# Kernel tuning notes

Hardware: AMD Instinct MI355X
Metric: run time of the kernel (lower is better)

## Reference

```python
import jax, jax.numpy as jnp
import numpy as np

B, T = 2, 2048
D_MODEL = 1024
N_LAYERS = 2
VOCAB = 256
BLOCK = 2048
LOCAL = 128
STRIDE = 256
NHEAD = D_MODEL // 64  # 16
HEAD_DIM = D_MODEL // NHEAD  # 64
LN_EPS = 1e-5


def setup_inputs() -> dict:
    key = jax.random.key(0)
    ks = jax.random.split(key, 16)
    L, d = N_LAYERS, D_MODEL

    def g(k, shape, scale=0.02):
        return (jax.random.normal(k, shape, dtype=jnp.float32) * scale)

    return {
        "x": jax.random.randint(ks[0], (B, T), 0, VOCAB),
        "embed": g(ks[1], (VOCAB, d)),
        "pos_embed": g(ks[2], (BLOCK, d)),
        # per-layer weights stacked on leading L axis; Linear as y = x @ W + b
        "Wq": g(ks[3], (L, d, d)), "bq": jnp.zeros((L, d), jnp.float32),
        "Wk": g(ks[4], (L, d, d)), "bk": jnp.zeros((L, d), jnp.float32),
        "Wv": g(ks[5], (L, d, d)), "bv": jnp.zeros((L, d), jnp.float32),
        "Wo": g(ks[6], (L, d, d)), "bo": jnp.zeros((L, d), jnp.float32),
        "g1": jnp.ones((L, d), jnp.float32), "be1": jnp.zeros((L, d), jnp.float32),
        "W1": g(ks[7], (L, d, 4 * d)), "bf1": jnp.zeros((L, 4 * d), jnp.float32),
        "W2": g(ks[8], (L, 4 * d, d)), "bf2": jnp.zeros((L, d), jnp.float32),
        "g2": jnp.ones((L, d), jnp.float32), "be2": jnp.zeros((L, d), jnp.float32),
        "gf": jnp.ones((d,), jnp.float32), "bef": jnp.zeros((d,), jnp.float32),
        "Whead": g(ks[9], (d, VOCAB)),
    }


def _ln(x, gamma, beta):
    mu = jnp.mean(x, axis=-1, keepdims=True)
    var = jnp.mean(jnp.square(x - mu), axis=-1, keepdims=True)
    return (x - mu) * jax.lax.rsqrt(var + LN_EPS) * gamma + beta


def _sparse_mask(t):
    # allowed[i, j] = True if token i may attend to token j
    i = jnp.arange(t)[:, None]
    j = jnp.arange(t)[None, :]
    causal = j <= i
    local = (i - j) <= LOCAL
    glob = (j % STRIDE) == 0
    return causal & (local | glob)


def _sparse_attn(q, k, v, allowed):
    # q, k, v: [B, T, D] -> [B, H, T, hd]
    b, t, d = q.shape
    def split(x):
        return x.reshape(b, t, NHEAD, HEAD_DIM).transpose(0, 2, 1, 3)
    q, k, v = split(q), split(k), split(v)
    scale = HEAD_DIM ** -0.5
    scores = jnp.einsum("bhqd,bhkd->bhqk", q, k) * scale
    scores = jnp.where(allowed[None, None], scores, -jnp.inf)
    attn = jax.nn.softmax(scores, axis=-1)  # every row has j=i allowed -> no NaN
    out = jnp.einsum("bhqk,bhkd->bhqd", attn, v)
    return out.transpose(0, 2, 1, 3).reshape(b, t, d)


def reference(x, embed, pos_embed, Wq, bq, Wk, bk, Wv, bv, Wo, bo,
              g1, be1, W1, bf1, W2, bf2, g2, be2, gf, bef, Whead):
    b, t = x.shape
    h = embed[x] + pos_embed[jnp.arange(t)][None]
    allowed = _sparse_mask(t)
    for l in range(N_LAYERS):
        h_n = _ln(h, g1[l], be1[l])
        q = h_n @ Wq[l] + bq[l]
        k = h_n @ Wk[l] + bk[l]
        v = h_n @ Wv[l] + bv[l]
        attn_out = _sparse_attn(q, k, v, allowed)
        h = h + (attn_out @ Wo[l] + bo[l])
        h2 = _ln(h, g2[l], be2[l])
        ffn = jax.nn.gelu(h2 @ W1[l] + bf1[l], approximate=False) @ W2[l] + bf2[l]
        h = h + ffn
    h = _ln(h, gf, bef)
    return h @ Whead
```

## Files before the change

### kernel.cpp

```cpp
#include <hip/hip_runtime.h>
#include <hip/hip_bf16.h>

#define BB 2
#define TT 2048
#define DD 1024
#define FF 4096
#define VV 256
#define HH 16
#define HD 64
#define MM (BB * TT)
#define LOCAL_W 128
#define STRIDE_G 256
#define QS 3072

typedef short s16x8 __attribute__((ext_vector_type(8)));
typedef __bf16 bf16x8 __attribute__((ext_vector_type(8)));
typedef float f32x4 __attribute__((ext_vector_type(4)));

#define WAITVM(N) asm volatile("s_waitcnt vmcnt(" #N ")" ::: "memory")
#define LGKM0 do { asm volatile("s_waitcnt lgkmcnt(0)" ::: "memory"); \
                   __builtin_amdgcn_sched_barrier(0); } while (0)

__device__ __forceinline__ float b2f(unsigned short u) {
  return __builtin_bit_cast(float, (unsigned int)u << 16);
}
__device__ __forceinline__ unsigned short f2b(float f) {
  __hip_bfloat16 h = __float2bfloat16(f);
  return __builtin_bit_cast(unsigned short, h);
}
__device__ __forceinline__ void gl_lds16(const unsigned short* g, unsigned short* l) {
  __builtin_amdgcn_global_load_lds(
      (const __attribute__((address_space(1))) void*)g,
      (__attribute__((address_space(3))) void*)l, 16, 0, 0);
}
__device__ __forceinline__ bf16x8 ldsr(const unsigned short* p) {
  return __builtin_bit_cast(bf16x8, *(const s16x8*)p);
}

__global__ __launch_bounds__(256) void transpose_k(const float* __restrict__ W,
                                                   unsigned short* __restrict__ WT,
                                                   int K, int N) {
  __shared__ float t[32][33];
  const int n0 = blockIdx.x * 32, k0 = blockIdx.y * 32;
  const int tx = threadIdx.x, ty = threadIdx.y;
  for (int r = ty; r < 32; r += 8) t[r][tx] = W[(size_t)(k0 + r) * N + n0 + tx];
  __syncthreads();
  for (int r = ty; r < 32; r += 8)
    WT[(size_t)(n0 + r) * K + k0 + tx] = f2b(t[tx][r]);
}

__global__ __launch_bounds__(256) void concat_bias(const float* __restrict__ bq,
                                                   const float* __restrict__ bk,
                                                   const float* __restrict__ bv,
                                                   float* __restrict__ bcat) {
  const int i = blockIdx.x * 256 + threadIdx.x;
  const int l = i / QS, j = i - l * QS;
  float v;
  if (j < DD) v = bq[l * DD + j];
  else if (j < 2 * DD) v = bk[l * DD + j - DD];
  else v = bv[l * DD + j - 2 * DD];
  bcat[i] = v;
}

__global__ __launch_bounds__(256) void embed_kernel(const int* __restrict__ x,
                                                    const float* __restrict__ emb,
                                                    const float* __restrict__ pos,
                                                    float* __restrict__ h) {
  const int row = blockIdx.x;
  const int c = threadIdx.x * 4;
  const int tok = x[row];
  const int t = row & (TT - 1);
  float4 e = *(const float4*)&emb[(size_t)tok * DD + c];
  float4 p = *(const float4*)&pos[(size_t)t * DD + c];
  e.x += p.x; e.y += p.y; e.z += p.z; e.w += p.w;
  *(float4*)&h[(size_t)row * DD + c] = e;
}

__global__ __launch_bounds__(256) void ln_kernel(const float* __restrict__ x,
                                                 const float* __restrict__ g,
                                                 const float* __restrict__ be,
                                                 unsigned short* __restrict__ out) {
  const int row = blockIdx.x;
  const int tid = threadIdx.x;
  const float4 v = *(const float4*)&x[(size_t)row * DD + tid * 4];
  float s = v.x + v.y + v.z + v.w;
  float sq = v.x * v.x + v.y * v.y + v.z * v.z + v.w * v.w;
#pragma unroll
  for (int off = 32; off; off >>= 1) {
    s += __shfl_xor(s, off);
    sq += __shfl_xor(sq, off);
  }
  __shared__ float ss[4], ssq[4];
  const int w = tid >> 6, lane = tid & 63;
  if (lane == 0) { ss[w] = s; ssq[w] = sq; }
  __syncthreads();
  s = ss[0] + ss[1] + ss[2] + ss[3];
  sq = ssq[0] + ssq[1] + ssq[2] + ssq[3];
  const float mean = s * (1.0f / DD);
  const float var = sq * (1.0f / DD) - mean * mean;
  const float rstd = rsqrtf(var + 1e-5f);
  const float4 gv = *(const float4*)&g[tid * 4];
  const float4 bv = *(const float4*)&be[tid * 4];
  ushort4 o;
  o.x = f2b((v.x - mean) * rstd * gv.x + bv.x);
  o.y = f2b((v.y - mean) * rstd * gv.y + bv.y);
  o.z = f2b((v.z - mean) * rstd * gv.z + bv.z);
  o.w = f2b((v.w - mean) * rstd * gv.w + bv.w);
  *(ushort4*)&out[(size_t)row * DD + tid * 4] = o;
}

__global__ __launch_bounds__(256) void ln_red(float* __restrict__ hio,
                                              const float* __restrict__ parts,
                                              const float* __restrict__ bias,
                                              const float* __restrict__ g,
                                              const float* __restrict__ be,
                                              unsigned short* __restrict__ out) {
  const int row = blockIdx.x;
  const int tid = threadIdx.x;
  const size_t base = (size_t)row * DD + tid * 4;
  f32x4 v = *(const f32x4*)&hio[base];
  v += *(const f32x4*)&bias[tid * 4];
  v += *(const f32x4*)&parts[base];
  v += *(const f32x4*)&parts[(size_t)MM * DD + base];
  *(f32x4*)&hio[base] = v;
  float s = v[0] + v[1] + v[2] + v[3];
  float sq = v[0] * v[0] + v[1] * v[1] + v[2] * v[2] + v[3] * v[3];
#pragma unroll
  for (int off = 32; off; off >>= 1) {
    s += __shfl_xor(s, off);
    sq += __shfl_xor(sq, off);
  }
  __shared__ float ss[4], ssq[4];
  const int w = tid >> 6, lane = tid & 63;
  if (lane == 0) { ss[w] = s; ssq[w] = sq; }
  __syncthreads();
  s = ss[0] + ss[1] + ss[2] + ss[3];
  sq = ssq[0] + ssq[1] + ssq[2] + ssq[3];
  const float mean = s * (1.0f / DD);
  const float var = sq * (1.0f / DD) - mean * mean;
  const float rstd = rsqrtf(var + 1e-5f);
  const float4 gv = *(const float4*)&g[tid * 4];
  const float4 bv = *(const float4*)&be[tid * 4];
  ushort4 o;
  o.x = f2b((v[0] - mean) * rstd * gv.x + bv.x);
  o.y = f2b((v[1] - mean) * rstd * gv.y + bv.y);
  o.z = f2b((v[2] - mean) * rstd * gv.z + bv.z);
  o.w = f2b((v[3] - mean) * rstd * gv.w + bv.w);
  *(ushort4*)&out[(size_t)row * DD + tid * 4] = o;
}

template <int EPI>
__global__ __launch_bounds__(512, 2) void gemm8p(const unsigned short* __restrict__ A,
                                                 const unsigned short* __restrict__ BT,
                                                 const float* __restrict__ bias,
                                                 unsigned short* __restrict__ outp,
                                                 int M, int N, int K, int nbx) {
  __shared__ __align__(16) unsigned short lds[65536];
  const int tid = threadIdx.x;
  const int lane = tid & 63;
  const int w = tid >> 6;
  const int nwg = gridDim.x;
  const int orig = blockIdx.x;
  const int wg = (orig & 7) * (nwg >> 3) + (orig >> 3);
  const int n0 = (wg % nbx) * 256, m0 = (wg / nbx) * 256;
  const int wm = w >> 2, wn = w & 3;
  f32x4 acc[8][4] = {};

  const unsigned short* aSrc[2];
  const unsigned short* bSrc[2];
  int dstO[2];
#pragma unroll
  for (int i = 0; i < 2; i++) {
    const int s = tid + (i << 9);
    const int row = s >> 2, sc = s & 3;
    const int l = sc ^ ((row >> 1) & 3);
    aSrc[i] = &A[(size_t)(m0 + row) * K + l * 8];
    bSrc[i] = &BT[(size_t)(n0 + row) * K + l * 8];
    dstO[i] = s * 8;
  }
  auto STAGE = [&](int tb, int ks, int obase) {
    const int kt = (tb << 6) + (ks << 5);
    const int so = obase + ks * 16384;
#pragma unroll
    for (int i = 0; i < 2; i++) {
      gl_lds16(aSrc[i] + kt, &lds[so + dstO[i]]);
      gl_lds16(bSrc[i] + kt, &lds[so + 8192 + dstO[i]]);
    }
  };

  const int rA = lane & 15, cr = lane >> 4;
  const int rowA0 = wm * 128 + rA;
  const int rowB0 = wn * 64 + rA;
  const int aAddr0 = rowA0 * 32 + ((cr ^ ((rowA0 >> 1) & 3)) << 3);
  const int bAddr0 = 8192 + rowB0 * 32 + ((cr ^ ((rowB0 >> 1) & 3)) << 3);

  const int NT = K >> 6;
  STAGE(0, 0, 0);
  STAGE(0, 1, 0);

  auto TILE = [&](int bufc, int tb, bool notlast) {
    const int bb = bufc << 15;
    const int ob = (bufc ^ 1) << 15;
    bf16x8 bfr[4], af[4];
    WAITVM(4);
    __builtin_amdgcn_s_barrier();
#pragma unroll
    for (int n = 0; n < 4; n++) bfr[n] = ldsr(&lds[bb + bAddr0 + n * 512]);
#pragma unroll
    for (int i = 0; i < 4; i++) af[i] = ldsr(&lds[bb + aAddr0 + i * 512]);
    if (notlast) STAGE(tb + 1, 0, ob);
    LGKM0;
    __builtin_amdgcn_s_setprio(1);
#pragma unroll
    for (int i = 0; i < 4; i++)
#pragma unroll
      for (int n = 0; n < 4; n++)
        acc[i][n] = __builtin_amdgcn_mfma_f32_16x16x32_bf16(af[i], bfr[n], acc[i][n], 0, 0, 0);
    __builtin_amdgcn_s_setprio(0);
#pragma unroll
    for (int i = 0; i < 4; i++) af[i] = ldsr(&lds[bb + aAddr0 + (4 + i) * 512]);
    LGKM0;
    __builtin_amdgcn_s_setprio(1);
#pragma unroll
    for (int i = 0; i < 4; i++)
#pragma unroll
      for (int n = 0; n < 4; n++)
        acc[4 + i][n] = __builtin_amdgcn_mfma_f32_16x16x32_bf16(af[i], bfr[n], acc[4 + i][n], 0, 0, 0);
    __builtin_amdgcn_s_setprio(0);
    if (notlast) { WAITVM(4); } else { WAITVM(0); }
    __builtin_amdgcn_s_barrier();
#pragma unroll
    for (int n = 0; n < 4; n++) bfr[n] = ldsr(&lds[bb + 16384 + bAddr0 + n * 512]);
#pragma unroll
    for (int i = 0; i < 4; i++) af[i] = ldsr(&lds[bb + 16384 + aAddr0 + i * 512]);
    if (notlast) STAGE(tb + 1, 1, ob);
    LGKM0;
    __builtin_amdgcn_s_setprio(1);
#pragma unroll
    for (int i = 0; i < 4; i++)
#pragma unroll
      for (int n = 0; n < 4; n++)
        acc[i][n] = __builtin_amdgcn_mfma_f32_16x16x32_bf16(af[i], bfr[n], acc[i][n], 0, 0, 0);
    __builtin_amdgcn_s_setprio(0);
#pragma unroll
    for (int i = 0; i < 4; i++) af[i] = ldsr(&lds[bb + 16384 + aAddr0 + (4 + i) * 512]);
    LGKM0;
    __builtin_amdgcn_s_setprio(1);
#pragma unroll
    for (int i = 0; i < 4; i++)
#pragma unroll
      for (int n = 0; n < 4; n++)
        acc[4 + i][n] = __builtin_amdgcn_mfma_f32_16x16x32_bf16(af[i], bfr[n], acc[4 + i][n], 0, 0, 0);
    __builtin_amdgcn_s_setprio(0);
  };

  for (int it = 0; it < NT; it += 2) {
    TILE(0, it, true);
    TILE(1, it + 1, it + 2 < NT);
  }

  const int r0 = (lane >> 4) * 4;
  const int cc = lane & 15;
#pragma unroll
  for (int m = 0; m < 8; m++) {
#pragma unroll
    for (int n = 0; n < 4; n++) {
#pragma unroll
      for (int r = 0; r < 4; r++) {
        const int row = m0 + wm * 128 + m * 16 + r0 + r;
        const int col = n0 + wn * 64 + n * 16 + cc;
        float val = acc[m][n][r] + bias[col];
        if (EPI == 3) {
          float u = val * (0.7978845608f + 0.0356774081f * val * val);
          u = fminf(u, 10.0f);
          const float e = __expf(2.0f * u);
          val = val * e / (e + 1.0f);
        }
        outp[(size_t)row * N + col] = f2b(val);
      }
    }
  }
}

__global__ __launch_bounds__(512, 2) void gemm_dw(const unsigned short* __restrict__ A,
                                                  const unsigned short* __restrict__ BT,
                                                  float* __restrict__ partial,
                                                  int M, int N, int K, int nbx, int nwg2,
                                                  int ksub) {
  __shared__ __align__(16) unsigned short lds[49152];
  const int tid = threadIdx.x;
  const int lane = tid & 63;
  const int w = tid >> 6;
  const int nwg = gridDim.x;
  const int orig = blockIdx.x;
  const int wg = (orig & 7) * (nwg >> 3) + (orig >> 3);
  const int ks = wg / nwg2;
  const int rem = wg - ks * nwg2;
  const int n0 = (rem % nbx) * 128;
  const int m0 = (rem / nbx) * 256;
  const int kb = ks * ksub;
  const int wm = w >> 2, wn = w & 3;
  f32x4 acc[8][2] = {};

  const unsigned short* aSrc[2];
  const unsigned short* bSrc;
  int dstA[2], dstB;
#pragma unroll
  for (int i = 0; i < 2; i++) {
    const int s = tid + (i << 9);
    const int row = s >> 2, sc = s & 3;
    const int l = sc ^ ((row >> 1) & 3);
    aSrc[i] = &A[(size_t)(m0 + row) * K + kb + l * 8];
    dstA[i] = s * 8;
  }
  {
    const int row = tid >> 2, sc = tid & 3;
    const int l = sc ^ ((row >> 1) & 3);
    bSrc = &BT[(size_t)(n0 + row) * K + kb + l * 8];
    dstB = 8192 + tid * 8;
  }
  auto STAGE = [&](int tb, int kss, int obase) {
    const int kt = (tb << 6) + (kss << 5);
    const int so = obase + kss * 12288;
    gl_lds16(aSrc[0] + kt, &lds[so + dstA[0]]);
    gl_lds16(aSrc[1] + kt, &lds[so + dstA[1]]);
    gl_lds16(bSrc + kt, &lds[so + dstB]);
  };

  const int rA = lane & 15, cr = lane >> 4;
  const int rowA0 = wm * 128 + rA;
  const int rowB0 = wn * 32 + rA;
  const int aAddr0 = rowA0 * 32 + ((cr ^ ((rowA0 >> 1) & 3)) << 3);
  const int bAddr0 = 8192 + rowB0 * 32 + ((cr ^ ((rowB0 >> 1) & 3)) << 3);

  const int NT = ksub >> 6;
  STAGE(0, 0, 0);
  STAGE(0, 1, 0);

  auto TILE = [&](int bufc, int tb, bool notlast) {
    const int bb = bufc * 24576;
    const int ob = (bufc ^ 1) * 24576;
    bf16x8 bfr[2], af[4];
    WAITVM(3);
    __builtin_amdgcn_s_barrier();
#pragma unroll
    for (int n = 0; n < 2; n++) bfr[n] = ldsr(&lds[bb + bAddr0 + n * 512]);
#pragma unroll
    for (int i = 0; i < 4; i++) af[i] = ldsr(&lds[bb + aAddr0 + i * 512]);
    if (notlast) STAGE(tb + 1, 0, ob);
    LGKM0;
    __builtin_amdgcn_s_setprio(1);
#pragma unroll
    for (int i = 0; i < 4; i++)
#pragma unroll
      for (int n = 0; n < 2; n++)
        acc[i][n] = __builtin_amdgcn_mfma_f32_16x16x32_bf16(af[i], bfr[n], acc[i][n], 0, 0, 0);
    __builtin_amdgcn_s_setprio(0);
#pragma unroll
    for (int i = 0; i < 4; i++) af[i] = ldsr(&lds[bb + aAddr0 + (4 + i) * 512]);
    LGKM0;
    __builtin_amdgcn_s_setprio(1);
#pragma unroll
    for (int i = 0; i < 4; i++)
#pragma unroll
      for (int n = 0; n < 2; n++)
        acc[4 + i][n] = __builtin_amdgcn_mfma_f32_16x16x32_bf16(af[i], bfr[n], acc[4 + i][n], 0, 0, 0);
    __builtin_amdgcn_s_setprio(0);
    if (notlast) { WAITVM(3); } else { WAITVM(0); }
    __builtin_amdgcn_s_barrier();
#pragma unroll
    for (int n = 0; n < 2; n++) bfr[n] = ldsr(&lds[bb + 12288 + bAddr0 + n * 512]);
#pragma unroll
    for (int i = 0; i < 4; i++) af[i] = ldsr(&lds[bb + 12288 + aAddr0 + i * 512]);
    if (notlast) STAGE(tb + 1, 1, ob);
    LGKM0;
    __builtin_amdgcn_s_setprio(1);
#pragma unroll
    for (int i = 0; i < 4; i++)
#pragma unroll
      for (int n = 0; n < 2; n++)
        acc[i][n] = __builtin_amdgcn_mfma_f32_16x16x32_bf16(af[i], bfr[n], acc[i][n], 0, 0, 0);
    __builtin_amdgcn_s_setprio(0);
#pragma unroll
    for (int i = 0; i < 4; i++) af[i] = ldsr(&lds[bb + 12288 + aAddr0 + (4 + i) * 512]);
    LGKM0;
    __builtin_amdgcn_s_setprio(1);
#pragma unroll
    for (int i = 0; i < 4; i++)
#pragma unroll
      for (int n = 0; n < 2; n++)
        acc[4 + i][n] = __builtin_amdgcn_mfma_f32_16x16x32_bf16(af[i], bfr[n], acc[4 + i][n], 0, 0, 0);
    __builtin_amdgcn_s_setprio(0);
  };

  for (int it = 0; it < NT; it += 2) {
    TILE(0, it, true);
    TILE(1, it + 1, it + 2 < NT);
  }

  float* pout = partial + (size_t)ks * M * N;
  const int r0 = (lane >> 4) * 4;
  const int cc = lane & 15;
#pragma unroll
  for (int m = 0; m < 8; m++)
#pragma unroll
    for (int n = 0; n < 2; n++)
#pragma unroll
      for (int r = 0; r < 4; r++) {
        const int row = m0 + wm * 128 + m * 16 + r0 + r;
        const int col = n0 + wn * 32 + n * 16 + cc;
        pout[(size_t)row * N + col] = acc[m][n][r];
      }
}

template <int EPI>
__global__ __launch_bounds__(512, 2) void gemm_p(const unsigned short* __restrict__ A,
                                                 const unsigned short* __restrict__ BT,
                                                 const float* __restrict__ bias,
                                                 const float* __restrict__ res,
                                                 void* __restrict__ outp,
                                                 int M, int N, int K, int nbx, int nwg2,
                                                 int ksub) {
  constexpr int BM = 128;
  __shared__ __align__(16) unsigned short lds[4][BM * 64];
  const int tid = threadIdx.x;
  const int lane = tid & 63;
  const int w = tid >> 6;
  const int nwg = gridDim.x;
  const int orig = blockIdx.x;
  const int wg = (orig & 7) * (nwg >> 3) + (orig >> 3);
  const int ks = wg / nwg2;
  const int rem = wg - ks * nwg2;
  const int n0 = (rem % nbx) * BM;
  const int m0 = (rem / nbx) * BM;
  const int kb = ks * ksub;
  const int wm = w >> 2, wn = w & 3;
  f32x4 acc[4][2] = {};

  auto STAGE = [&](int t) {
    const int b = t & 3;
    const int kt = kb + (t << 5);
    const int s = tid;
    const int row = s >> 2, sc = s & 3;
    const int c = sc ^ ((row >> 1) & 3);
    gl_lds16(&A[(size_t)(m0 + row) * K + kt + c * 8], &lds[b][s * 8]);
    gl_lds16(&BT[(size_t)(n0 + row) * K + kt + c * 8], &lds[b][BM * 32 + s * 8]);
  };

  const int NT = ksub >> 5;
  STAGE(0); STAGE(1); STAGE(2);

  for (int t = 0; t < NT; ++t) {
    const int ahead = NT - 1 - t;
    if (ahead >= 2) WAITVM(4); else if (ahead == 1) WAITVM(2); else WAITVM(0);
    __builtin_amdgcn_s_barrier();
    asm volatile("" ::: "memory");
    if (t + 3 < NT) STAGE(t + 3);
    const int b = t & 3;
    const int rA = lane & 15, cr = lane >> 4;
    bf16x8 af[4], bfr[2];
#pragma unroll
    for (int m = 0; m < 4; m++) {
      const int row = wm * 64 + m * 16 + rA;
      af[m] = ldsr(&lds[b][row * 32 + ((cr ^ ((row >> 1) & 3)) << 3)]);
    }
#pragma unroll
    for (int n = 0; n < 2; n++) {
      const int row = wn * 32 + n * 16 + rA;
      bfr[n] = ldsr(&lds[b][BM * 32 + row * 32 + ((cr ^ ((row >> 1) & 3)) << 3)]);
    }
    __builtin_amdgcn_s_setprio(1);
#pragma unroll
    for (int m = 0; m < 4; m++)
#pragma unroll
      for (int n = 0; n < 2; n++)
        acc[m][n] = __builtin_amdgcn_mfma_f32_16x16x32_bf16(af[m], bfr[n], acc[m][n], 0, 0, 0);
    __builtin_amdgcn_s_setprio(0);
  }

  const int r0 = (lane >> 4) * 4;
  const int cc = lane & 15;
  float* pout = (EPI == 0) ? ((float*)outp + (size_t)ks * M * N) : (float*)outp;
#pragma unroll
  for (int m = 0; m < 4; m++) {
#pragma unroll
    for (int n = 0; n < 2; n++) {
#pragma unroll
      for (int r = 0; r < 4; r++) {
        const int row = m0 + wm * 64 + m * 16 + r0 + r;
        const int col = n0 + wn * 32 + n * 16 + cc;
        const size_t idx = (size_t)row * N + col;
        if (EPI == 0) {
          pout[idx] = acc[m][n][r];
        } else {
          ((float*)outp)[idx] = acc[m][n][r] + bias[col] + res[idx];
        }
      }
    }
  }
}

template <int NP>
__global__ __launch_bounds__(256) void reduce_k(float* __restrict__ dst,
                                                const float* __restrict__ parts,
                                                size_t total) {
  const size_t i = ((size_t)blockIdx.x * 256 + threadIdx.x) * 4;
  if (i >= total) return;
  f32x4 acc = {};
#pragma unroll
  for (int p = 0; p < NP; p++) acc += *(const f32x4*)&parts[(size_t)p * total + i];
  *(f32x4*)&dst[i] = acc;
}

#define QT 16
#define KT 32
#define NTMAX 6
#define KP 72
#define PP 40

__global__ __launch_bounds__(256) void attn_mfma(const unsigned short* __restrict__ qkv,
                                                 unsigned short* __restrict__ outg) {
  __shared__ __align__(16) unsigned short kvs[4][KT * KP];
  __shared__ __align__(16) unsigned short pls[4][QT * PP];
  const int tid = threadIdx.x;
  const int wid = tid >> 6, lane = tid & 63;
  const int qgrp = blockIdx.x & 31;
  const int bh = blockIdx.x >> 5;
  const int h = bh & (HH - 1), b = bh >> 4;
  const size_t baseq = (size_t)b * TT * QS + (size_t)h * HD;
  const size_t baseo = (size_t)b * TT * DD + (size_t)h * HD;
  const int i0 = qgrp * 64 + wid * 16;
  const int g = lane >> 4;
  const int c = lane & 15;

  const int i0b = qgrp * 64 + 48;
  const int ka0b = (i0b > 128) ? ((i0b - 128) & ~31) : 0;
  const int nlb = ((i0b + 16 - ka0b) + 31) >> 5;
  const int neb = (ka0b + 255) >> 8;
  const int ka0 = (i0 > 128) ? ((i0 - 128) & ~31) : 0;
  const int ne = (ka0 + 255) >> 8;

  const s16x8 qf0 = *(const s16x8*)&qkv[baseq + (size_t)(i0 + c) * QS + g * 8];
  const s16x8 qf1 = *(const s16x8*)&qkv[baseq + (size_t)(i0 + c) * QS + 32 + g * 8];

  f32x4 sc[NTMAX][2];
  float smax[4] = {-1e30f, -1e30f, -1e30f, -1e30f};

#pragma unroll
  for (int t = 0; t < NTMAX; t++) {
    if (t > nlb) continue;
    const bool isg = (t == 0);
    if (isg && neb == 0) continue;
    const int kt0 = ka0 + (t - 1) * 32;
#pragma unroll
    for (int it = 0; it < 4; it++) {
      const int row = it * 8 + (lane >> 3);
      const int ch = lane & 7;
      const int j = isg ? ((row < ne) ? row * STRIDE_G : 0) : (kt0 + row);
      *(s16x8*)&kvs[wid][row * KP + ch * 8] =
          *(const s16x8*)&qkv[baseq + DD + (size_t)j * QS + ch * 8];
    }
    __syncthreads();
#pragma unroll
    for (int half = 0; half < 2; half++) {
      const int key = half * 16 + c;
      const bf16x8 kb0 = __builtin_bit_cast(bf16x8, *(const s16x8*)&kvs[wid][key * KP + g * 8]);
      const bf16x8 kb1 = __builtin_bit_cast(bf16x8, *(const s16x8*)&kvs[wid][key * KP + 32 + g * 8]);
      f32x4 a = {};
      a = __builtin_amdgcn_mfma_f32_16x16x32_bf16(__builtin_bit_cast(bf16x8, qf0), kb0, a, 0, 0, 0);
      a = __builtin_amdgcn_mfma_f32_16x16x32_bf16(__builtin_bit_cast(bf16x8, qf1), kb1, a, 0, 0, 0);
#pragma unroll
      for (int r = 0; r < 4; r++) {
        const int i = i0 + g * 4 + r;
        bool ok;
        if (isg) {
          ok = (key < ne);
        } else {
          const int j = kt0 + key;
          ok = (j <= i) && (((i - j) <= LOCAL_W) || ((j & (STRIDE_G - 1)) == 0));
        }
        const float s = ok ? a[r] * 0.125f : -1e30f;
        sc[t][half][r] = s;
        smax[r] = fmaxf(smax[r], s);
      }
    }
    __syncthreads();
  }
#pragma unroll
  for (int r = 0; r < 4; r++)
#pragma unroll
    for (int off = 8; off; off >>= 1)
      smax[r] = fmaxf(smax[r], __shfl_xor(smax[r], off));

  f32x4 o[4] = {};
  float lsum[4] = {0.f, 0.f, 0.f, 0.f};
#pragma unroll
  for (int t = 0; t < NTMAX; t++) {
    if (t > nlb) continue;
    const bool isg = (t == 0);
    if (isg && neb == 0) continue;
    const int kt0 = ka0 + (t - 1) * 32;
#pragma unroll
    for (int it = 0; it < 4; it++) {
      const int row = it * 8 + (lane >> 3);
      const int ch = lane & 7;
      const int j = isg ? ((row < ne) ? row * STRIDE_G : 0) : (kt0 + row);
      *(s16x8*)&kvs[wid][row * KP + ch * 8] =
          *(const s16x8*)&qkv[baseq + 2 * DD + (size_t)j * QS + ch * 8];
    }
#pragma unroll
    for (int half = 0; half < 2; half++)
#pragma unroll
      for (int r = 0; r < 4; r++) {
        const float p = __expf(sc[t][half][r] - smax[r]);
        lsum[r] += p;
        pls[wid][(g * 4 + r) * PP + half * 16 + c] = f2b(p);
      }
    __syncthreads();
    const bf16x8 pa = __builtin_bit_cast(bf16x8, *(const s16x8*)&pls[wid][c * PP + g * 8]);
#pragma unroll
    for (int d0 = 0; d0 < 4; d0++) {
      s16x8 bv;
#pragma unroll
      for (int e = 0; e < 8; e++)
        bv[e] = (short)kvs[wid][(g * 8 + e) * KP + d0 * 16 + c];
      o[d0] = __builtin_amdgcn_mfma_f32_16x16x32_bf16(pa, __builtin_bit_cast(bf16x8, bv), o[d0], 0, 0, 0);
    }
    __syncthreads();
  }
#pragma unroll
  for (int r = 0; r < 4; r++)
#pragma unroll
    for (int off = 8; off; off >>= 1)
      lsum[r] += __shfl_xor(lsum[r], off);
#pragma unroll
  for (int d0 = 0; d0 < 4; d0++)
#pragma unroll
    for (int r = 0; r < 4; r++)
      outg[baseo + (size_t)(i0 + g * 4 + r) * DD + d0 * 16 + c] = f2b(o[d0][r] / lsum[r]);
}

extern "C" void kernel_launch(void* const* d_in, const int* in_sizes, int n_in,
                              void* d_out, int out_size, void* d_ws, size_t ws_size,
                              hipStream_t stream) {
  const int* x = (const int*)d_in[0];
  const float* embed = (const float*)d_in[1];
  const float* pos = (const float*)d_in[2];
  const float* Wq = (const float*)d_in[3];
  const float* bq = (const float*)d_in[4];
  const float* Wk = (const float*)d_in[5];
  const float* bk = (const float*)d_in[6];
  const float* Wv = (const float*)d_in[7];
  const float* bv = (const float*)d_in[8];
  const float* Wo = (const float*)d_in[9];
  const float* bo = (const float*)d_in[10];
  const float* g1 = (const float*)d_in[11];
  const float* be1 = (const float*)d_in[12];
  const float* W1 = (const float*)d_in[13];
  const float* bf1 = (const float*)d_in[14];
  const float* W2 = (const float*)d_in[15];
  const float* bf2 = (const float*)d_in[16];
  const float* g2 = (const float*)d_in[17];
  const float* be2 = (const float*)d_in[18];
  const float* gf = (const float*)d_in[19];
  const float* bef = (const float*)d_in[20];
  const float* Whead = (const float*)d_in[21];

  char* ws = (char*)d_ws;
  size_t off = 0;
  auto alloc = [&](size_t bytes) -> void* {
    void* p = ws + off;
    off += (bytes + 255) & ~(size_t)255;
    return p;
  };
  unsigned short* WqkvT = (unsigned short*)alloc((size_t)2 * QS * DD * 2);
  unsigned short* WoT = (unsigned short*)alloc((size_t)2 * DD * DD * 2);
  unsigned short* W1T = (unsigned short*)alloc((size_t)2 * DD * FF * 2);
  unsigned short* W2T = (unsigned short*)alloc((size_t)2 * DD * FF * 2);
  unsigned short* WheadT = (unsigned short*)alloc((size_t)DD * VV * 2);
  float* bcat = (float*)alloc((size_t)2 * QS * 4);
  float* h = (float*)alloc((size_t)MM * DD * 4);
  unsigned short* hn = (unsigned short*)alloc((size_t)MM * DD * 2);
  unsigned short* qkvb = (unsigned short*)alloc((size_t)MM * QS * 2);
  unsigned short* attnb = (unsigned short*)alloc((size_t)MM * DD * 2);
  unsigned short* mid = (unsigned short*)alloc((size_t)MM * FF * 2);
  float* ffn2p = (float*)qkvb;
  float* headp = (float*)mid;
  (void)ws_size;

  const dim3 tb(32, 8);
  for (int l = 0; l < 2; l++) {
    const size_t wo = (size_t)l * DD * DD;
    const size_t wf = (size_t)l * DD * FF;
    transpose_k<<<dim3(DD / 32, DD / 32), tb, 0, stream>>>(Wq + wo, WqkvT + (size_t)l * QS * DD, DD, DD);
    transpose_k<<<dim3(DD / 32, DD / 32), tb, 0, stream>>>(Wk + wo, WqkvT + ((size_t)l * QS + DD) * DD, DD, DD);
    transpose_k<<<dim3(DD / 32, DD / 32), tb, 0, stream>>>(Wv + wo, WqkvT + ((size_t)l * QS + 2 * DD) * DD, DD, DD);
    transpose_k<<<dim3(DD / 32, DD / 32), tb, 0, stream>>>(Wo + wo, WoT + wo, DD, DD);
    transpose_k<<<dim3(FF / 32, DD / 32), tb, 0, stream>>>(W1 + wf, W1T + wf, DD, FF);
    transpose_k<<<dim3(DD / 32, FF / 32), tb, 0, stream>>>(W2 + wf, W2T + wf, FF, DD);
  }
  transpose_k<<<dim3(VV / 32, DD / 32), tb, 0, stream>>>(Whead, WheadT, DD, VV);
  concat_bias<<<24, 256, 0, stream>>>(bq, bk, bv, bcat);

  embed_kernel<<<MM, 256, 0, stream>>>(x, embed, pos, h);
  ln_kernel<<<MM, 256, 0, stream>>>(h, g1, be1, hn);

  for (int l = 0; l < 2; l++) {
    const size_t wo = (size_t)l * DD * DD;
    const size_t wf = (size_t)l * DD * FF;
    gemm8p<1><<<(QS / 256) * (MM / 256), 512, 0, stream>>>(
        hn, WqkvT + (size_t)l * QS * DD, bcat + l * QS, qkvb, MM, QS, DD, QS / 256);
    attn_mfma<<<BB * HH * (TT / 64), 256, 0, stream>>>(qkvb, attnb);
    gemm_p<2><<<(DD / 128) * (MM / 128), 512, 0, stream>>>(
        attnb, WoT + wo, bo + l * DD, h, h,
        MM, DD, DD, DD / 128, (DD / 128) * (MM / 128), DD);
    ln_kernel<<<MM, 256, 0, stream>>>(h, g2 + l * DD, be2 + l * DD, hn);
    gemm8p<3><<<(FF / 256) * (MM / 256), 512, 0, stream>>>(
        hn, W1T + wf, bf1 + l * FF, mid, MM, FF, DD, FF / 256);
    gemm_dw<<<2 * (DD / 128) * (MM / 256), 512, 0, stream>>>(
        mid, W2T + wf, ffn2p, MM, DD, FF, DD / 128, (DD / 128) * (MM / 256), FF / 2);
    if (l == 0)
      ln_red<<<MM, 256, 0, stream>>>(h, ffn2p, bf2, g1 + DD, be1 + DD, hn);
    else
      ln_red<<<MM, 256, 0, stream>>>(h, ffn2p, bf2 + DD, gf, bef, hn);
  }
  gemm_p<0><<<4 * (VV / 128) * (MM / 128), 512, 0, stream>>>(
      hn, WheadT, nullptr, nullptr, headp,
      MM, VV, DD, VV / 128, (VV / 128) * (MM / 128), DD / 4);
  reduce_k<4><<<(MM * VV) / 1024, 256, 0, stream>>>(
      (float*)d_out, headp, (size_t)MM * VV);
}
```

Before: 438.6 us.

## Issue next-tile prefetch before LDS reads and split-K the output projection

In the gemm8p and gemm_dw main loops, the global-to-LDS prefetch for the next tile is now issued immediately after the barrier, ahead of the LDS fragment reads. The explicit lgkmcnt(0) waits and sched_barriers are removed so the compiler can schedule LDS reads and MFMAs more freely. The attention output projection moves from gemm_p with a fused bias+residual epilogue to a 2-way split-K gemm_dw writing fp32 partials. Bias, residual and LayerNorm are then applied together in ln_red, which replaces the separate ln_kernel. This trades extra partial-buffer traffic for more workgroups and one less kernel. It relies on compiler-inserted waits for correctness of the LDS reads.

```diff
diff --git a/kernel.cpp b/kernel.cpp
--- a/kernel.cpp
+++ b/kernel.cpp
@@ -18,8 +18,7 @@
 typedef float f32x4 __attribute__((ext_vector_type(4)));
 
 #define WAITVM(N) asm volatile("s_waitcnt vmcnt(" #N ")" ::: "memory")
-#define LGKM0 do { asm volatile("s_waitcnt lgkmcnt(0)" ::: "memory"); \
-                   __builtin_amdgcn_sched_barrier(0); } while (0)
+#define CFENCE asm volatile("" ::: "memory")
 
 __device__ __forceinline__ float b2f(unsigned short u) {
   return __builtin_bit_cast(float, (unsigned int)u << 16);
@@ -204,12 +203,12 @@
     bf16x8 bfr[4], af[4];
     WAITVM(4);
     __builtin_amdgcn_s_barrier();
+    CFENCE;
+    if (notlast) STAGE(tb + 1, 0, ob);
 #pragma unroll
     for (int n = 0; n < 4; n++) bfr[n] = ldsr(&lds[bb + bAddr0 + n * 512]);
 #pragma unroll
     for (int i = 0; i < 4; i++) af[i] = ldsr(&lds[bb + aAddr0 + i * 512]);
-    if (notlast) STAGE(tb + 1, 0, ob);
-    LGKM0;
     __builtin_amdgcn_s_setprio(1);
 #pragma unroll
     for (int i = 0; i < 4; i++)
@@ -219,7 +218,6 @@
     __builtin_amdgcn_s_setprio(0);
 #pragma unroll
     for (int i = 0; i < 4; i++) af[i] = ldsr(&lds[bb + aAddr0 + (4 + i) * 512]);
-    LGKM0;
     __builtin_amdgcn_s_setprio(1);
 #pragma unroll
     for (int i = 0; i < 4; i++)
@@ -229,12 +227,12 @@
     __builtin_amdgcn_s_setprio(0);
     if (notlast) { WAITVM(4); } else { WAITVM(0); }
     __builtin_amdgcn_s_barrier();
+    CFENCE;
+    if (notlast) STAGE(tb + 1, 1, ob);
 #pragma unroll
     for (int n = 0; n < 4; n++) bfr[n] = ldsr(&lds[bb + 16384 + bAddr0 + n * 512]);
 #pragma unroll
     for (int i = 0; i < 4; i++) af[i] = ldsr(&lds[bb + 16384 + aAddr0 + i * 512]);
-    if (notlast) STAGE(tb + 1, 1, ob);
-    LGKM0;
     __builtin_amdgcn_s_setprio(1);
 #pragma unroll
     for (int i = 0; i < 4; i++)
@@ -244,7 +242,6 @@
     __builtin_amdgcn_s_setprio(0);
 #pragma unroll
     for (int i = 0; i < 4; i++) af[i] = ldsr(&lds[bb + 16384 + aAddr0 + (4 + i) * 512]);
-    LGKM0;
     __builtin_amdgcn_s_setprio(1);
 #pragma unroll
     for (int i = 0; i < 4; i++)
@@ -343,12 +340,12 @@
     bf16x8 bfr[2], af[4];
     WAITVM(3);
     __builtin_amdgcn_s_barrier();
+    CFENCE;
+    if (notlast) STAGE(tb + 1, 0, ob);
 #pragma unroll
     for (int n = 0; n < 2; n++) bfr[n] = ldsr(&lds[bb + bAddr0 + n * 512]);
 #pragma unroll
     for (int i = 0; i < 4; i++) af[i] = ldsr(&lds[bb + aAddr0 + i * 512]);
-    if (notlast) STAGE(tb + 1, 0, ob);
-    LGKM0;
     __builtin_amdgcn_s_setprio(1);
 #pragma unroll
     for (int i = 0; i < 4; i++)
@@ -358,7 +355,6 @@
     __builtin_amdgcn_s_setprio(0);
 #pragma unroll
     for (int i = 0; i < 4; i++) af[i] = ldsr(&lds[bb + aAddr0 + (4 + i) * 512]);
-    LGKM0;
     __builtin_amdgcn_s_setprio(1);
 #pragma unroll
     for (int i = 0; i < 4; i++)
@@ -368,12 +364,12 @@
     __builtin_amdgcn_s_setprio(0);
     if (notlast) { WAITVM(3); } else { WAITVM(0); }
     __builtin_amdgcn_s_barrier();
+    CFENCE;
+    if (notlast) STAGE(tb + 1, 1, ob);
 #pragma unroll
     for (int n = 0; n < 2; n++) bfr[n] = ldsr(&lds[bb + 12288 + bAddr0 + n * 512]);
 #pragma unroll
     for (int i = 0; i < 4; i++) af[i] = ldsr(&lds[bb + 12288 + aAddr0 + i * 512]);
-    if (notlast) STAGE(tb + 1, 1, ob);
-    LGKM0;
     __builtin_amdgcn_s_setprio(1);
 #pragma unroll
     for (int i = 0; i < 4; i++)
@@ -383,7 +379,6 @@
     __builtin_amdgcn_s_setprio(0);
 #pragma unroll
     for (int i = 0; i < 4; i++) af[i] = ldsr(&lds[bb + 12288 + aAddr0 + (4 + i) * 512]);
-    LGKM0;
     __builtin_amdgcn_s_setprio(1);
 #pragma unroll
     for (int i = 0; i < 4; i++)
@@ -413,12 +408,9 @@
       }
 }
 
-template <int EPI>
 __global__ __launch_bounds__(512, 2) void gemm_p(const unsigned short* __restrict__ A,
                                                  const unsigned short* __restrict__ BT,
-                                                 const float* __restrict__ bias,
-                                                 const float* __restrict__ res,
-                                                 void* __restrict__ outp,
+                                                 float* __restrict__ outp,
                                                  int M, int N, int K, int nbx, int nwg2,
                                                  int ksub) {
   constexpr int BM = 128;
@@ -454,7 +446,7 @@
     const int ahead = NT - 1 - t;
     if (ahead >= 2) WAITVM(4); else if (ahead == 1) WAITVM(2); else WAITVM(0);
     __builtin_amdgcn_s_barrier();
-    asm volatile("" ::: "memory");
+    CFENCE;
     if (t + 3 < NT) STAGE(t + 3);
     const int b = t & 3;
     const int rA = lane & 15, cr = lane >> 4;
@@ -480,24 +472,17 @@
 
   const int r0 = (lane >> 4) * 4;
   const int cc = lane & 15;
-  float* pout = (EPI == 0) ? ((float*)outp + (size_t)ks * M * N) : (float*)outp;
-#pragma unroll
-  for (int m = 0; m < 4; m++) {
-#pragma unroll
-    for (int n = 0; n < 2; n++) {
+  float* pout = outp + (size_t)ks * M * N;
+#pragma unroll
+  for (int m = 0; m < 4; m++)
+#pragma unroll
+    for (int n = 0; n < 2; n++)
 #pragma unroll
       for (int r = 0; r < 4; r++) {
         const int row = m0 + wm * 64 + m * 16 + r0 + r;
         const int col = n0 + wn * 32 + n * 16 + cc;
-        const size_t idx = (size_t)row * N + col;
-        if (EPI == 0) {
-          pout[idx] = acc[m][n][r];
-        } else {
-          ((float*)outp)[idx] = acc[m][n][r] + bias[col] + res[idx];
-        }
+        pout[(size_t)row * N + col] = acc[m][n][r];
       }
-    }
-  }
 }
 
 template <int NP>
@@ -685,6 +670,7 @@
   unsigned short* attnb = (unsigned short*)alloc((size_t)MM * DD * 2);
   unsigned short* mid = (unsigned short*)alloc((size_t)MM * FF * 2);
   float* ffn2p = (float*)qkvb;
+  float* oprojp = (float*)mid;
   float* headp = (float*)mid;
   (void)ws_size;
 
@@ -711,10 +697,9 @@
     gemm8p<1><<<(QS / 256) * (MM / 256), 512, 0, stream>>>(
         hn, WqkvT + (size_t)l * QS * DD, bcat + l * QS, qkvb, MM, QS, DD, QS / 256);
     attn_mfma<<<BB * HH * (TT / 64), 256, 0, stream>>>(qkvb, attnb);
-    gemm_p<2><<<(DD / 128) * (MM / 128), 512, 0, stream>>>(
-        attnb, WoT + wo, bo + l * DD, h, h,
-        MM, DD, DD, DD / 128, (DD / 128) * (MM / 128), DD);
-    ln_kernel<<<MM, 256, 0, stream>>>(h, g2 + l * DD, be2 + l * DD, hn);
+    gemm_dw<<<2 * (DD / 128) * (MM / 256), 512, 0, stream>>>(
+        attnb, WoT + wo, oprojp, MM, DD, DD, DD / 128, (DD / 128) * (MM / 256), DD / 2);
+    ln_red<<<MM, 256, 0, stream>>>(h, oprojp, bo + l * DD, g2 + l * DD, be2 + l * DD, hn);
     gemm8p<3><<<(FF / 256) * (MM / 256), 512, 0, stream>>>(
         hn, W1T + wf, bf1 + l * FF, mid, MM, FF, DD, FF / 256);
     gemm_dw<<<2 * (DD / 128) * (MM / 256), 512, 0, stream>>>(
@@ -724,9 +709,8 @@
     else
       ln_red<<<MM, 256, 0, stream>>>(h, ffn2p, bf2 + DD, gf, bef, hn);
   }
-  gemm_p<0><<<4 * (VV / 128) * (MM / 128), 512, 0, stream>>>(
-      hn, WheadT, nullptr, nullptr, headp,
-      MM, VV, DD, VV / 128, (VV / 128) * (MM / 128), DD / 4);
+  gemm_p<<<4 * (VV / 128) * (MM / 128), 512, 0, stream>>>(
+      hn, WheadT, headp, MM, VV, DD, VV / 128, (VV / 128) * (MM / 128), DD / 4);
   reduce_k<4><<<(MM * VV) / 1024, 256, 0, stream>>>(
       (float*)d_out, headp, (size_t)MM * VV);
 }
```

After: 440.7 us. No clear change (+0.5%).
